# Performance work log

Hardware: AMD Instinct MI355X
Metric: run time of the kernel (lower is better)

Reference implementation:

```python
import jax, jax.numpy as jnp
import numpy as np

B, N, IN_DIM, OUT_DIM, H = 8, 1024, 256, 256, 4
D = OUT_DIM // H  # head_dim = 64
NEG_INF = -9e15
LRELU_SLOPE = 0.2


def setup_inputs() -> dict:
    key = jax.random.key(0)
    k1, k2, k3, k4 = jax.random.split(key, 4)
    x = jax.random.normal(k1, (B, N, IN_DIM), dtype=jnp.float32)
    adj = jax.random.randint(k2, (B, N, N), 0, 2).astype(jnp.float32)
    # xavier-ish scaled params
    W = jax.random.normal(k3, (IN_DIM, H * D), dtype=jnp.float32) * jnp.sqrt(2.0 / (IN_DIM + H * D))
    a = jax.random.normal(k4, (H, 2 * D), dtype=jnp.float32) * jnp.sqrt(2.0 / (H + 2 * D))
    return {"x": x, "adj": adj, "W": W, "a": a}


def reference(x, adj, W, a):
    # h = W(x): (B, N, H*D) -> (B, H, N, D)
    h = jnp.einsum('bni,io->bno', x, W).reshape(x.shape[0], x.shape[1], H, D)
    h = h.transpose(0, 2, 1, 3)  # bhnd
    # e_ij = a . concat(h_i, h_j) = a1.h_i + a2.h_j  (no NxN x 2D concat materialized)
    a1, a2 = a[:, :D], a[:, D:]
    e_i = jnp.einsum('bhnd,hd->bhn', h, a1)  # source term
    e_j = jnp.einsum('bhmd,hd->bhm', h, a2)  # target term
    e = e_i[:, :, :, None] + e_j[:, :, None, :]  # (B, H, N, N)
    e = jnp.where(e > 0, e, LRELU_SLOPE * e)  # LeakyReLU(0.2)
    # mask by adjacency, softmax over neighbors (last axis)
    e = jnp.where(adj[:, None, :, :] > 0, e, NEG_INF)
    attn = jax.nn.softmax(e, axis=-1)  # dropout is identity at eval
    # weighted sum of neighbor features
    out = jnp.einsum('bhnm,bhmd->bhnd', attn, h)
    # concat heads: (B, N, H*D)
    out = out.transpose(0, 2, 1, 3).reshape(x.shape[0], x.shape[1], H * D)
    return out
```

## Files before the change

kernel.cpp:

```cpp
#include <hip/hip_runtime.h>
#include <hip/hip_bf16.h>
#include <stdint.h>

typedef float f32x4 __attribute__((ext_vector_type(4)));
typedef short s16x8 __attribute__((ext_vector_type(8)));
typedef unsigned short u16x4 __attribute__((ext_vector_type(4)));

#define LOG2E 1.4426950408889634f

__device__ inline unsigned short f2bf(float f){
    __hip_bfloat16 h = __float2bfloat16(f);
    return __builtin_bit_cast(unsigned short, h);
}
__device__ inline float bf2f(unsigned short u){
    unsigned v = ((unsigned)u) << 16;
    return __builtin_bit_cast(float, v);
}
__device__ inline float exp2_fast(float x){
#if __has_builtin(__builtin_amdgcn_exp2f)
    return __builtin_amdgcn_exp2f(x);
#else
    float r; asm volatile("v_exp_f32 %0, %1\n\ts_nop 0\n\ts_nop 0" : "=v"(r) : "v"(x)); return r;
#endif
}
__device__ inline void gld_lds16(const void* g, void* l){
    __builtin_amdgcn_global_load_lds((const __attribute__((address_space(1))) unsigned*)g,
                                     (__attribute__((address_space(3))) unsigned*)l, 16, 0, 0);
}

__global__ __launch_bounds__(256) void k_wt(const float* __restrict__ W,
                                            unsigned short* __restrict__ Wt){
    int c = blockIdx.x, k = threadIdx.x;
    Wt[c*256 + k] = f2bf(W[k*256 + c]);
}

__global__ __launch_bounds__(256) void k_gemm(const float* __restrict__ x,
                                              const unsigned short* __restrict__ Wt,
                                              unsigned short* __restrict__ hT){
    __shared__ unsigned short trans[64][68];
    int orig = blockIdx.x;
    int swz  = (orig & 7)*64 + (orig >> 3);
    int rbi = swz >> 2, cbi = swz & 3;
    int tid = threadIdx.x;
    int w = tid >> 6, lane = tid & 63;
    int r16 = lane & 15, kq = lane >> 4;

    const float*          xp = x  + (size_t)((rbi*64 + w*16 + r16)*256 + kq*8);
    const unsigned short* wp = Wt + (size_t)((cbi*64 + r16)*256 + kq*8);

    f32x4 acc[4] = {{0,0,0,0},{0,0,0,0},{0,0,0,0},{0,0,0,0}};
    #pragma unroll
    for (int ks=0; ks<8; ++ks){
        f32x4 xa = *(const f32x4*)(xp + ks*32);
        f32x4 xb = *(const f32x4*)(xp + ks*32 + 4);
        s16x8 af;
        af[0]=(short)f2bf(xa[0]); af[1]=(short)f2bf(xa[1]);
        af[2]=(short)f2bf(xa[2]); af[3]=(short)f2bf(xa[3]);
        af[4]=(short)f2bf(xb[0]); af[5]=(short)f2bf(xb[1]);
        af[6]=(short)f2bf(xb[2]); af[7]=(short)f2bf(xb[3]);
        #pragma unroll
        for (int t=0;t<4;++t){
            s16x8 bf = *(const s16x8*)(wp + t*16*256 + ks*32);
            acc[t] = __builtin_amdgcn_mfma_f32_16x16x32_bf16(af, bf, acc[t], 0,0,0);
        }
    }
    #pragma unroll
    for (int t=0;t<4;++t)
        #pragma unroll
        for (int j=0;j<4;++j)
            trans[t*16 + r16][w*16 + kq*4 + j] = f2bf(acc[t][j]);
    __syncthreads();
    int d = tid & 63, seg = tid >> 6;
    int b  = rbi >> 4;
    int n0 = (rbi & 15) * 64;
    unsigned short* dst = hT + ((size_t)((b*4 + cbi)*64 + d))*1024 + n0 + seg*16;
    #pragma unroll
    for (int q=0;q<4;++q){
        u16x4 v = *(const u16x4*)&trans[d][seg*16 + q*4];
        *(u16x4*)(dst + q*4) = v;
    }
}

__global__ __launch_bounds__(256) void k_ev(const unsigned short* __restrict__ hT,
                                            const float* __restrict__ a,
                                            float* __restrict__ ei, float* __restrict__ ej,
                                            float* __restrict__ mj){
    int bh = blockIdx.x;
    int h  = bh & 3;
    int tid = threadIdx.x;
    const unsigned short* base = hT + (size_t)bh*64*1024 + tid*4;
    float acc1[4] = {0,0,0,0}, acc2[4] = {0,0,0,0};
    for (int d=0; d<64; ++d){
        float va1 = a[h*128 + d];
        float va2 = a[h*128 + 64 + d];
        u16x4 v = *(const u16x4*)(base + (size_t)d*1024);
        #pragma unroll
        for (int i=0;i<4;++i){
            float f = bf2f(v[i]);
            acc1[i] = __builtin_fmaf(f, va1, acc1[i]);
            acc2[i] = __builtin_fmaf(f, va2, acc2[i]);
        }
    }
    #pragma unroll
    for (int i=0;i<4;++i){
        ei[bh*1024 + tid*4 + i] = acc1[i];
        ej[bh*1024 + tid*4 + i] = acc2[i];
    }
    float lmax = fmaxf(fmaxf(acc2[0],acc2[1]), fmaxf(acc2[2],acc2[3]));
    #pragma unroll
    for (int off=32; off; off>>=1) lmax = fmaxf(lmax, __shfl_xor(lmax, off));
    __shared__ float red[4];
    if ((tid & 63)==0) red[tid>>6] = lmax;
    __syncthreads();
    if (tid==0) mj[bh] = fmaxf(fmaxf(red[0],red[1]), fmaxf(red[2],red[3]));
}

__global__ __launch_bounds__(256) void k_attn(const float* __restrict__ adj,
                                              const unsigned short* __restrict__ hT,
                                              const float* __restrict__ ei,
                                              const float* __restrict__ ejg,
                                              const float* __restrict__ mj,
                                              float* __restrict__ out){
    __shared__ alignas(16) unsigned short slab[2][64*64];
    __shared__ alignas(16) float ejs[1024];
    int orig = blockIdx.x;
    int swz  = (orig & 7)*64 + (orig >> 3);
    int bh = swz >> 4, qi = swz & 15;
    int b = bh >> 2, h = bh & 3;
    int tid = threadIdx.x, w = tid >> 6, lane = tid & 63;
    int r16 = lane & 15, kq = lane >> 4;
    int qb = qi*64;
    int nrow = qb + w*16 + r16;

    *(f32x4*)(ejs + tid*4) = *(const f32x4*)(ejg + bh*1024 + tid*4);

    float eir = ei[bh*1024 + nrow];
    float s0  = eir + mj[bh];
    float stab2 = fmaxf(s0, 0.2f*s0) * LOG2E;

    const unsigned short* hTb  = hT + (size_t)bh*64*1024;
    const float* adjrow        = adj + ((size_t)(b*1024 + nrow))*1024;

    f32x4 acc[4] = {{0,0,0,0},{0,0,0,0},{0,0,0,0},{0,0,0,0}};
    float rs = 0.f;

    auto stage = [&](int buf, int ms){
        int m0 = ms*64;
        #pragma unroll
        for (int c=0;c<2;++c){
            int dd = c*32 + (tid >> 3);
            int ck = (tid & 7) ^ (dd & 7);
            const unsigned short* src = hTb + (size_t)dd*1024 + m0 + ck*8;
            char* ldst = (char*)&slab[buf][0] + c*4096 + w*1024;
            gld_lds16(src, ldst);
        }
    };

    stage(0, 0);
    __syncthreads();
    for (int ms=0; ms<16; ++ms){
        int cur = ms & 1;
        if (ms < 15) stage(cur^1, ms+1);
        int m0 = ms*64;
        #pragma unroll
        for (int kb=0; kb<2; ++kb){
            const float* ap = adjrow + m0 + kb*32 + kq*8;
            f32x4 ad0 = *(const f32x4*)ap;
            f32x4 ad1 = *(const f32x4*)(ap + 4);
            const float* ejp = ejs + m0 + kb*32 + kq*8;
            f32x4 ej0 = *(const f32x4*)ejp;
            f32x4 ej1 = *(const f32x4*)(ejp + 4);
            s16x8 pf;
            float pv[8];
            #pragma unroll
            for (int j=0;j<8;++j){
                float ejv = (j<4) ? ej0[j] : ej1[j-4];
                float av  = (j<4) ? ad0[j] : ad1[j-4];
                float s  = eir + ejv;
                float t2 = fmaxf(s, 0.2f*s);
                float e  = exp2_fast(__builtin_fmaf(t2, LOG2E, -stab2));
                unsigned short pb = f2bf(av * e);
                pf[j] = (short)pb;
                pv[j] = bf2f(pb);
            }
            rs += ((pv[0]+pv[1])+(pv[2]+pv[3])) + ((pv[4]+pv[5])+(pv[6]+pv[7]));
            #pragma unroll
            for (int t=0;t<4;++t){
                int dd = t*16 + r16;
                int co = (kb*4 + kq) ^ (dd & 7);
                s16x8 bf = *(const s16x8*)(&slab[cur][0] + dd*64 + co*8);
                acc[t] = __builtin_amdgcn_mfma_f32_16x16x32_bf16(pf, bf, acc[t], 0,0,0);
            }
        }
        __syncthreads();
    }

    rs += __shfl_xor(rs, 16);
    rs += __shfl_xor(rs, 32);
    #pragma unroll
    for (int j=0;j<4;++j){
        float rsj = __shfl(rs, kq*4 + j);
        float inv = 1.0f / rsj;
        int n = qb + w*16 + kq*4 + j;
        float* op = out + ((size_t)(b*1024 + n))*256 + h*64 + r16;
        #pragma unroll
        for (int t=0;t<4;++t)
            op[t*16] = acc[t][j] * inv;
    }
}

extern "C" void kernel_launch(void* const* d_in, const int* in_sizes, int n_in,
                              void* d_out, int out_size, void* d_ws, size_t ws_size,
                              hipStream_t stream){
    const float* x   = (const float*)d_in[0];
    const float* adj = (const float*)d_in[1];
    const float* W   = (const float*)d_in[2];
    const float* a   = (const float*)d_in[3];
    float* out = (float*)d_out;
    char* ws = (char*)d_ws;
    unsigned short* Wt = (unsigned short*)ws;
    unsigned short* hT = (unsigned short*)(ws + (128<<10));
    float* ei = (float*)(ws + (128<<10) + (4<<20));
    float* ej = ei + 32768;
    float* mj = ej + 32768;

    k_wt  <<<256, 256, 0, stream>>>(W, Wt);
    k_gemm<<<512, 256, 0, stream>>>(x, Wt, hT);
    k_ev  <<<32,  256, 0, stream>>>(hT, a, ei, ej, mj);
    k_attn<<<512, 256, 0, stream>>>(adj, hT, ei, ej, mj, out);
}
```

Measured before the change: 50.13 us.

## Bit-pack adjacency once, fuse attention logits into GEMM, drop max stabilization

A new kernel packs the fp32 adjacency matrix into 64-bit ballot masks once per row. The attention kernel then reads those bits instead of re-reading the full fp32 adjacency for each of the four heads. The per-node source and target logit projections move into the GEMM epilogue, with the log2e scale folded in, so the separate k_ev launch goes away. Softmax max-stabilization is dropped and the row-sum denominator is clamped. This relies on the logits being small enough that exp2 does not overflow.

```diff
diff --git a/kernel.cpp b/kernel.cpp
--- a/kernel.cpp
+++ b/kernel.cpp
@@ -34,10 +34,29 @@
     Wt[c*256 + k] = f2bf(W[k*256 + c]);
 }
 
+__global__ __launch_bounds__(256) void k_adjbits(const float* __restrict__ adj,
+                                                 unsigned long long* __restrict__ abits){
+    int w = threadIdx.x >> 6, lane = threadIdx.x & 63;
+    int row = blockIdx.x*4 + w;
+    const float* src = adj + (size_t)row*1024 + lane;
+    unsigned long long my = 0;
+    #pragma unroll
+    for (int ms=0; ms<16; ++ms){
+        float v = src[ms*64];
+        unsigned long long m = __ballot(v != 0.0f);
+        if (lane == ms) my = m;
+    }
+    if (lane < 16) abits[(size_t)row*16 + lane] = my;
+}
+
 __global__ __launch_bounds__(256) void k_gemm(const float* __restrict__ x,
                                               const unsigned short* __restrict__ Wt,
-                                              unsigned short* __restrict__ hT){
+                                              const float* __restrict__ a,
+                                              unsigned short* __restrict__ hT,
+                                              float* __restrict__ eiL,
+                                              float* __restrict__ ejL){
     __shared__ unsigned short trans[64][68];
+    __shared__ float red[2][4][64];
     int orig = blockIdx.x;
     int swz  = (orig & 7)*64 + (orig >> 3);
     int rbi = swz >> 2, cbi = swz & 3;
@@ -70,76 +89,65 @@
         for (int j=0;j<4;++j)
             trans[t*16 + r16][w*16 + kq*4 + j] = f2bf(acc[t][j]);
     __syncthreads();
-    int d = tid & 63, seg = tid >> 6;
+
     int b  = rbi >> 4;
     int n0 = (rbi & 15) * 64;
-    unsigned short* dst = hT + ((size_t)((b*4 + cbi)*64 + d))*1024 + n0 + seg*16;
-    #pragma unroll
-    for (int q=0;q<4;++q){
-        u16x4 v = *(const u16x4*)&trans[d][seg*16 + q*4];
-        *(u16x4*)(dst + q*4) = v;
-    }
-}
-
-__global__ __launch_bounds__(256) void k_ev(const unsigned short* __restrict__ hT,
-                                            const float* __restrict__ a,
-                                            float* __restrict__ ei, float* __restrict__ ej,
-                                            float* __restrict__ mj){
-    int bh = blockIdx.x;
-    int h  = bh & 3;
-    int tid = threadIdx.x;
-    const unsigned short* base = hT + (size_t)bh*64*1024 + tid*4;
-    float acc1[4] = {0,0,0,0}, acc2[4] = {0,0,0,0};
-    for (int d=0; d<64; ++d){
-        float va1 = a[h*128 + d];
-        float va2 = a[h*128 + 64 + d];
-        u16x4 v = *(const u16x4*)(base + (size_t)d*1024);
-        #pragma unroll
-        for (int i=0;i<4;++i){
-            float f = bf2f(v[i]);
-            acc1[i] = __builtin_fmaf(f, va1, acc1[i]);
-            acc2[i] = __builtin_fmaf(f, va2, acc2[i]);
-        }
-    }
-    #pragma unroll
-    for (int i=0;i<4;++i){
-        ei[bh*1024 + tid*4 + i] = acc1[i];
-        ej[bh*1024 + tid*4 + i] = acc2[i];
-    }
-    float lmax = fmaxf(fmaxf(acc2[0],acc2[1]), fmaxf(acc2[2],acc2[3]));
-    #pragma unroll
-    for (int off=32; off; off>>=1) lmax = fmaxf(lmax, __shfl_xor(lmax, off));
-    __shared__ float red[4];
-    if ((tid & 63)==0) red[tid>>6] = lmax;
+
+    {
+        int d = tid & 63, seg = tid >> 6;
+        unsigned short* dst = hT + ((size_t)((b*4 + cbi)*64 + d))*1024 + n0 + seg*16;
+        #pragma unroll
+        for (int q=0;q<4;++q){
+            u16x4 v = *(const u16x4*)&trans[d][seg*16 + q*4];
+            *(u16x4*)(dst + q*4) = v;
+        }
+    }
+
+    {
+        int seg = tid >> 6, n = tid & 63;
+        const float* ap = a + cbi*128;
+        float p1 = 0.f, p2 = 0.f;
+        #pragma unroll
+        for (int q=0;q<16;++q){
+            int dd = seg*16 + q;
+            float hv = bf2f(trans[dd][n]);
+            p1 = __builtin_fmaf(hv, ap[dd],    p1);
+            p2 = __builtin_fmaf(hv, ap[64+dd], p2);
+        }
+        red[0][seg][n] = p1;
+        red[1][seg][n] = p2;
+    }
     __syncthreads();
-    if (tid==0) mj[bh] = fmaxf(fmaxf(red[0],red[1]), fmaxf(red[2],red[3]));
-}
-
-__global__ __launch_bounds__(256) void k_attn(const float* __restrict__ adj,
+    if (tid < 128){
+        int which = tid >> 6, nn = tid & 63;
+        float s = red[which][0][nn] + red[which][1][nn] + red[which][2][nn] + red[which][3][nn];
+        float* dst = which ? ejL : eiL;
+        dst[(size_t)(b*4 + cbi)*1024 + n0 + nn] = s * LOG2E;
+    }
+}
+
+__global__ __launch_bounds__(256) void k_attn(const uint2* __restrict__ abits,
                                               const unsigned short* __restrict__ hT,
-                                              const float* __restrict__ ei,
-                                              const float* __restrict__ ejg,
-                                              const float* __restrict__ mj,
+                                              const float* __restrict__ eiL,
+                                              const float* __restrict__ ejLg,
                                               float* __restrict__ out){
     __shared__ alignas(16) unsigned short slab[2][64*64];
     __shared__ alignas(16) float ejs[1024];
     int orig = blockIdx.x;
     int swz  = (orig & 7)*64 + (orig >> 3);
     int bh = swz >> 4, qi = swz & 15;
-    int b = bh >> 2, h = bh & 3;
+    int b = bh >> 2;
     int tid = threadIdx.x, w = tid >> 6, lane = tid & 63;
-    int r16 = lane & 15, kq = lane >> 4;
+    int r16 = lane & 15, kq = lane >> 4, kq8 = kq*8;
     int qb = qi*64;
     int nrow = qb + w*16 + r16;
 
-    *(f32x4*)(ejs + tid*4) = *(const f32x4*)(ejg + bh*1024 + tid*4);
-
-    float eir = ei[bh*1024 + nrow];
-    float s0  = eir + mj[bh];
-    float stab2 = fmaxf(s0, 0.2f*s0) * LOG2E;
-
-    const unsigned short* hTb  = hT + (size_t)bh*64*1024;
-    const float* adjrow        = adj + ((size_t)(b*1024 + nrow))*1024;
+    *(f32x4*)(ejs + tid*4) = *(const f32x4*)(ejLg + bh*1024 + tid*4);
+
+    float eirL = eiL[bh*1024 + nrow];
+
+    const unsigned short* hTb = hT + (size_t)bh*64*1024;
+    const uint2* abrow        = abits + ((size_t)(b*1024 + nrow))*16;
 
     f32x4 acc[4] = {{0,0,0,0},{0,0,0,0},{0,0,0,0},{0,0,0,0}};
     float rs = 0.f;
@@ -156,18 +164,19 @@
         }
     };
 
+    uint2 abcur = abrow[0];
     stage(0, 0);
     __syncthreads();
     for (int ms=0; ms<16; ++ms){
         int cur = ms & 1;
-        if (ms < 15) stage(cur^1, ms+1);
-        int m0 = ms*64;
+        uint2 abnext = abcur;
+        if (ms < 15){ stage(cur^1, ms+1); abnext = abrow[ms+1]; }
+        unsigned wlo = abcur.x >> kq8;
+        unsigned whi = abcur.y >> kq8;
         #pragma unroll
         for (int kb=0; kb<2; ++kb){
-            const float* ap = adjrow + m0 + kb*32 + kq*8;
-            f32x4 ad0 = *(const f32x4*)ap;
-            f32x4 ad1 = *(const f32x4*)(ap + 4);
-            const float* ejp = ejs + m0 + kb*32 + kq*8;
+            unsigned word = kb ? whi : wlo;
+            const float* ejp = ejs + ms*64 + kb*32 + kq8;
             f32x4 ej0 = *(const f32x4*)ejp;
             f32x4 ej1 = *(const f32x4*)(ejp + 4);
             s16x8 pf;
@@ -175,11 +184,11 @@
             #pragma unroll
             for (int j=0;j<8;++j){
                 float ejv = (j<4) ? ej0[j] : ej1[j-4];
-                float av  = (j<4) ? ad0[j] : ad1[j-4];
-                float s  = eir + ejv;
-                float t2 = fmaxf(s, 0.2f*s);
-                float e  = exp2_fast(__builtin_fmaf(t2, LOG2E, -stab2));
-                unsigned short pb = f2bf(av * e);
+                float sL = eirL + ejv;
+                float t  = fmaxf(sL, 0.2f*sL);
+                float e  = exp2_fast(t);
+                float bitf = (float)((word >> j) & 1u);
+                unsigned short pb = f2bf(bitf * e);
                 pf[j] = (short)pb;
                 pv[j] = bf2f(pb);
             }
@@ -193,14 +202,16 @@
             }
         }
         __syncthreads();
+        abcur = abnext;
     }
 
     rs += __shfl_xor(rs, 16);
     rs += __shfl_xor(rs, 32);
+    int h = bh & 3;
     #pragma unroll
     for (int j=0;j<4;++j){
         float rsj = __shfl(rs, kq*4 + j);
-        float inv = 1.0f / rsj;
+        float inv = 1.0f / fmaxf(rsj, 1e-30f);
         int n = qb + w*16 + kq*4 + j;
         float* op = out + ((size_t)(b*1024 + n))*256 + h*64 + r16;
         #pragma unroll
@@ -220,12 +231,12 @@
     char* ws = (char*)d_ws;
     unsigned short* Wt = (unsigned short*)ws;
     unsigned short* hT = (unsigned short*)(ws + (128<<10));
-    float* ei = (float*)(ws + (128<<10) + (4<<20));
-    float* ej = ei + 32768;
-    float* mj = ej + 32768;
-
-    k_wt  <<<256, 256, 0, stream>>>(W, Wt);
-    k_gemm<<<512, 256, 0, stream>>>(x, Wt, hT);
-    k_ev  <<<32,  256, 0, stream>>>(hT, a, ei, ej, mj);
-    k_attn<<<512, 256, 0, stream>>>(adj, hT, ei, ej, mj, out);
-}
+    float* eiL = (float*)(ws + (128<<10) + (4<<20));
+    float* ejL = eiL + 32768;
+    unsigned long long* abits = (unsigned long long*)(ws + (128<<10) + (4<<20) + (256<<10));
+
+    k_wt     <<<256,  256, 0, stream>>>(W, Wt);
+    k_adjbits<<<2048, 256, 0, stream>>>(adj, abits);
+    k_gemm   <<<512,  256, 0, stream>>>(x, Wt, a, hT, eiL, ejL);
+    k_attn   <<<512,  256, 0, stream>>>((const uint2*)abits, hT, eiL, ejL, out);
+}
```

Measured after the change: 49.61 us. Within noise of the previous version (-1.0%).
